# Performance work log

Measured on AMD Instinct MI355X. Metric: run time of the kernel, lower is better.

Reference implementation:

```python
import jax, jax.numpy as jnp
import numpy as np

EPS = 1e-5  # GraphNorm eps


def setup_inputs() -> dict:
    key = jax.random.key(0)
    ks = jax.random.split(key, 8)
    B, N, D, L = 8, 2048, 128, 3
    return {
        "instance": jax.random.uniform(ks[0], (B, N, 2), jnp.float32),
        "Wn": jax.random.normal(ks[1], (D, 2), jnp.float32) * 0.5,
        "bn": jnp.zeros((D,), jnp.float32),
        "Wg": jax.random.normal(ks[2], (L, D, D), jnp.float32) / np.sqrt(D).astype(np.float32),
        "bg": jnp.zeros((L, D), jnp.float32),
        "gn_w": jnp.ones((D,), jnp.float32),
        "gn_b": jnp.zeros((D,), jnp.float32),
        "gn_a": jnp.ones((D,), jnp.float32),
    }


def reference(instance, Wn, bn, Wg, bg, gn_w, gn_b, gn_a):
    # instance: [B, N, 2] city coordinates. Graph is complete, so the PyG
    # edge-list GCN over all (i != j) pairs + self-loops is exactly a dense
    # symmetric-normalized adjacency matmul per graph.
    B, N, _ = instance.shape
    # pairwise Euclidean distances (cdist), safe sqrt to keep diagonal exact 0
    sq = jnp.sum(instance * instance, axis=-1)                      # [B, N]
    d2 = sq[:, :, None] + sq[:, None, :] - 2.0 * jnp.einsum(
        'bnd,bmd->bnm', instance, instance)                          # [B, N, N]
    pos = d2 > 0
    dist = jnp.where(pos, jnp.sqrt(jnp.where(pos, d2, 1.0)), 0.0)    # [B, N, N]
    # GCN edge weights = distances, self-loops added with weight 1.0
    A = dist + jnp.eye(N, dtype=dist.dtype)
    deg = jnp.sum(A, axis=-1)                                        # [B, N]
    dinv = jax.lax.rsqrt(deg)
    An = dinv[:, :, None] * A * dinv[:, None, :]                     # D^-1/2 A D^-1/2

    h = jnp.einsum('bne,de->bnd', instance, Wn) + bn                 # proj_node
    for l in range(Wg.shape[0]):
        # GCNConv: aggregate normalized messages of lin(x), then bias
        hw = jnp.einsum('bnm,bmd->bnd', An, jnp.einsum('bnd,ed->bne', h, Wg[l])) + bg[l]
        h = jnp.tanh(hw) + h                                         # activation + residual
        # GraphNorm (shared params across layers): per-graph, per-feature stats
        mean = jnp.mean(h, axis=1, keepdims=True)                    # [B, 1, D]
        sub = h - gn_a * mean
        var = jnp.mean(sub * sub, axis=1, keepdims=True)
        h = gn_w * sub * jax.lax.rsqrt(var + EPS) + gn_b
    return h  # [B, N, D] (unbatch+stack of equal-size graphs)
```

## Files before the change

kernel.cpp:

```cpp
#include <hip/hip_runtime.h>
#include <hip/hip_bf16.h>
#include <math.h>

#define BB 8
#define NN 2048
#define DD 128
#define LL 3
#define GN_EPS 1e-5f

typedef __attribute__((ext_vector_type(8))) short bf16x8;
typedef __attribute__((ext_vector_type(4))) float f32x4;
typedef __attribute__((ext_vector_type(8))) unsigned short u16x8;

#define FSQRT(x) __builtin_amdgcn_sqrtf(x)

__device__ __forceinline__ unsigned short f2bf(float f) {
    union { float f; unsigned u; } v; v.f = f;
    return (unsigned short)((v.u + 0x8000u) >> 16);
}

__device__ __forceinline__ float fast_tanh(float x) {
    float e = __expf(-2.0f * fabsf(x));
    float t = (1.0f - e) * __builtin_amdgcn_rcpf(1.0f + e);
    return copysignf(t, x);
}

__device__ __forceinline__ void stats_sc(float ps, float pq, float a, float w_,
                                         float b_, float& s, float& c) {
    const float inv_n = 1.0f / (float)NN;
    float mean = ps * inv_n;
    float msq  = pq * inv_n;
    float var  = msq - mean * mean * a * (2.0f - a);
    float rstd = rsqrtf(var + GN_EPS);
    s = w_ * rstd;
    c = b_ - s * (a * mean);
}


__global__ __launch_bounds__(256)
void gen_pack(const float* __restrict__ inst, const float* __restrict__ Wn,
              const float* __restrict__ bn, const float* __restrict__ Wg,
              unsigned short* __restrict__ wgf,
              float* __restrict__ dinv, float* __restrict__ h,
              unsigned short* __restrict__ tp,
              float* __restrict__ psum, float* __restrict__ psq)
{
    __shared__ float cs[NN * 2];
    __shared__ float part[4][16];
    __shared__ float weffL[2 * DD], beffL[DD];
    const int b     = blockIdx.x & 7;
    const int ntile = blockIdx.x >> 3;
    const int n0    = ntile * 16;
    const int tid   = threadIdx.x;
    const int w     = tid >> 6;
    const int lane  = tid & 63;
    const int lq    = lane >> 4;
    const int ll    = lane & 15;

    if (blockIdx.x < 192) {
        const int f = blockIdx.x * 256 + tid;
        const int l  = f >> 14;
        const int r  = f & 16383;
        const int dp = r >> 7;
        const int e  = r & 127;
        const int dpt = dp >> 4, llp = dp & 15;
        const int kc  = e >> 5,  eo = e & 31;
        wgf[((((l * 8 + dpt) * 4 + kc) * 16 + llp) << 5) + eo] = f2bf(Wg[f]);
    }

    const float* instb = inst + b * NN * 2;
    for (int i = tid; i < (NN * 2) / 4; i += 256)
        ((float4*)cs)[i] = ((const float4*)instb)[i];

    if (tid < DD) {
        const int ee = tid;
        float a0 = 0.f, a1 = 0.f, cc = 0.f;
        for (int d = 0; d < 128; ++d) {
            const float wv = Wg[ee * 128 + d];
            a0 = fmaf(wv, Wn[d * 2 + 0], a0);
            a1 = fmaf(wv, Wn[d * 2 + 1], a1);
            cc = fmaf(wv, bn[d], cc);
        }
        weffL[ee * 2 + 0] = a0;
        weffL[ee * 2 + 1] = a1;
        beffL[ee] = cc;
    }
    __syncthreads();

    const int n = n0 + ll;
    const float nx = cs[n * 2 + 0];
    const float ny = cs[n * 2 + 1];

    const int diagkcg = ntile >> 1;
    float rs = 0.f;
    for (int kc = 0; kc < 16; ++kc) {
        const int kcg = w * 16 + kc;
        const int mb  = kcg * 32 + lq * 8;
        const float* cp = &cs[mb * 2];
        float4 c01 = *(const float4*)(cp + 0);
        float4 c23 = *(const float4*)(cp + 4);
        float4 c45 = *(const float4*)(cp + 8);
        float4 c67 = *(const float4*)(cp + 12);
        float mxx[8] = { c01.x, c01.z, c23.x, c23.z, c45.x, c45.z, c67.x, c67.z };
        float myy[8] = { c01.y, c01.w, c23.y, c23.w, c45.y, c45.w, c67.y, c67.w };
        float dist[8];
        #pragma unroll
        for (int j = 0; j < 8; ++j) {
            float dx = nx - mxx[j];
            float dy = ny - myy[j];
            dist[j] = FSQRT(dx * dx + dy * dy);
        }
        if (kcg == diagkcg) {
            #pragma unroll
            for (int j = 0; j < 8; ++j)
                if (mb + j == n) dist[j] = 1.0f;
        }
        #pragma unroll
        for (int j = 0; j < 8; ++j) rs += dist[j];
    }

    rs += __shfl_xor(rs, 16);
    rs += __shfl_xor(rs, 32);
    if (lq == 0) part[w][ll] = rs;
    __syncthreads();
    if (tid < 16)
        dinv[b * NN + n0 + tid] = rsqrtf(part[0][tid] + part[1][tid] +
                                         part[2][tid] + part[3][tid]);

    {
        const int d  = tid & 127;
        const int r0 = tid >> 7;
        const float w0 = Wn[d * 2 + 0];
        const float w1 = Wn[d * 2 + 1];
        const float bv = bn[d];
        const float we0 = weffL[d * 2 + 0];
        const float we1 = weffL[d * 2 + 1];
        const float be  = beffL[d];
        const int kcg   = ntile >> 1;
        const int mbase = (ntile & 1) * 16;
        const int dt    = d >> 4;
        const int lld   = d & 15;
        unsigned short* tpd =
            tp + (((size_t)(b * 64 + kcg) * 8 + dt) * 64 + lld) * 8;
        #pragma unroll
        for (int r = r0; r < 16; r += 2) {
            const float x0 = cs[(n0 + r) * 2 + 0];
            const float x1 = cs[(n0 + r) * 2 + 1];
            h[((size_t)b * NN + n0 + r) * DD + d] = fmaf(x0, w0, fmaf(x1, w1, bv));
            const float dv = rsqrtf(part[0][r] + part[1][r] + part[2][r] + part[3][r]);
            const int mloc = mbase + r;
            const int lqa  = mloc >> 3;
            const int j    = mloc & 7;
            tpd[(size_t)lqa * 128 + j] = f2bf(dv * fmaf(x0, we0, fmaf(x1, we1, be)));
        }
    }
    if (blockIdx.x == 0) {
        for (int i = tid; i < LL * BB * DD; i += 256) { psum[i] = 0.f; psq[i] = 0.f; }
    }
}

template <bool HP>
__global__ __launch_bounds__(256)
void lin_mfma(const float* __restrict__ h, const unsigned short* __restrict__ wgf_l,
              const float* __restrict__ dinv,
              const float* __restrict__ psumP, const float* __restrict__ psqP,
              const float* __restrict__ ga, const float* __restrict__ gw,
              const float* __restrict__ gb, unsigned short* __restrict__ tp)
{
    __shared__ float sL[DD], cL[DD];
    const int tid  = threadIdx.x;
    const int b    = blockIdx.x & 7;
    const int tile = blockIdx.x >> 3;
    const int row0 = b * NN + tile * 32;
    const int w    = tid >> 6;
    const int lane = tid & 63;
    const int lq   = lane >> 4;
    const int ll   = lane & 15;

    if (tid < DD) {
        float s = 1.0f, c = 0.0f;
        if (HP)
            stats_sc(psumP[b * DD + tid], psqP[b * DD + tid],
                     ga[tid], gw[tid], gb[tid], s, c);
        sL[tid] = s; cL[tid] = c;
    }
    __syncthreads();

    bf16x8 aw[2][4];
    #pragma unroll
    for (int mt = 0; mt < 2; ++mt) {
        const int dpt = 2 * w + mt;
        #pragma unroll
        for (int kc = 0; kc < 4; ++kc)
            aw[mt][kc] = *(const bf16x8*)&wgf_l[(((dpt * 4 + kc) * 16 + ll) << 5) + lq * 8];
    }

    bf16x8 bh[2][4];
    #pragma unroll
    for (int nt = 0; nt < 2; ++nt) {
        const float* hrow = h + (size_t)(row0 + nt * 16 + ll) * DD;
        #pragma unroll
        for (int kc = 0; kc < 4; ++kc) {
            float4 h0 = *(const float4*)&hrow[kc * 32 + lq * 8];
            float4 h1 = *(const float4*)&hrow[kc * 32 + lq * 8 + 4];
            const int e0 = kc * 32 + lq * 8;
            bf16x8 p;
            p[0] = (short)f2bf(fmaf(sL[e0 + 0], h0.x, cL[e0 + 0]));
            p[1] = (short)f2bf(fmaf(sL[e0 + 1], h0.y, cL[e0 + 1]));
            p[2] = (short)f2bf(fmaf(sL[e0 + 2], h0.z, cL[e0 + 2]));
            p[3] = (short)f2bf(fmaf(sL[e0 + 3], h0.w, cL[e0 + 3]));
            p[4] = (short)f2bf(fmaf(sL[e0 + 4], h1.x, cL[e0 + 4]));
            p[5] = (short)f2bf(fmaf(sL[e0 + 5], h1.y, cL[e0 + 5]));
            p[6] = (short)f2bf(fmaf(sL[e0 + 6], h1.z, cL[e0 + 6]));
            p[7] = (short)f2bf(fmaf(sL[e0 + 7], h1.w, cL[e0 + 7]));
            bh[nt][kc] = p;
        }
    }

    f32x4 acc[2][2];
    #pragma unroll
    for (int i = 0; i < 2; ++i)
        #pragma unroll
        for (int j = 0; j < 2; ++j) acc[i][j] = (f32x4)0.0f;

    #pragma unroll
    for (int kc = 0; kc < 4; ++kc)
        #pragma unroll
        for (int nt = 0; nt < 2; ++nt)
            #pragma unroll
            for (int mt = 0; mt < 2; ++mt)
                acc[nt][mt] = __builtin_amdgcn_mfma_f32_16x16x32_bf16(
                    bh[nt][kc], aw[mt][kc], acc[nt][mt], 0, 0, 0);

    #pragma unroll
    for (int nt = 0; nt < 2; ++nt) {
        const int mloc0 = nt * 16 + lq * 4;
        const int lq_a  = mloc0 >> 3;
        const int j0    = mloc0 & 7;
        float4 di4 = *(const float4*)&dinv[row0 + mloc0];
        #pragma unroll
        for (int mt = 0; mt < 2; ++mt) {
            const int dt = 2 * w + mt;
            ushort4 pk;
            pk.x = f2bf(acc[nt][mt][0] * di4.x);
            pk.y = f2bf(acc[nt][mt][1] * di4.y);
            pk.z = f2bf(acc[nt][mt][2] * di4.z);
            pk.w = f2bf(acc[nt][mt][3] * di4.w);
            *(ushort4*)&tp[((size_t)((b * 64 + tile) * 8 + dt) * 64 + lq_a * 16 + ll) * 8 + j0] = pk;
        }
    }
}

template <bool HP>
__global__ __launch_bounds__(256, 4)
void agg_mfma(const float* __restrict__ inst, const unsigned short* __restrict__ tp,
              const float* __restrict__ dinv, const float* __restrict__ bg_l,
              const float* __restrict__ psumP, const float* __restrict__ psqP,
              const float* __restrict__ ga, const float* __restrict__ gw,
              const float* __restrict__ gb,
              float* __restrict__ h, float* __restrict__ psum, float* __restrict__ psq)
{
    __shared__ __align__(16) char shm[32768];
    float* cs = (float*)shm;
    const int b     = blockIdx.x & 7;
    const int ntile = blockIdx.x >> 3;
    const int n0    = ntile * 16;
    const int tid   = threadIdx.x;
    const int w     = tid >> 6;
    const int lane  = tid & 63;
    const int lq    = lane >> 4;
    const int ll    = lane & 15;

    const float* instb = inst + b * NN * 2;
    for (int i = tid; i < (NN * 2) / 4; i += 256)
        ((float4*)cs)[i] = ((const float4*)instb)[i];

    const unsigned short* tpb = tp + ((size_t)b * 64 * 8) * 512 + lane * 8;

    f32x4 acc[8];
    #pragma unroll
    for (int dt = 0; dt < 8; ++dt) acc[dt] = (f32x4)0.0f;

    bf16x8 fb[8];

    __syncthreads();

    const int   nr = n0 + ll;
    const float nx = cs[nr * 2 + 0], ny = cs[nr * 2 + 1];
    const int diagk = ntile >> 1;
    const int kcg0  = w * 16;

    #pragma unroll
    for (int kc = 0; kc < 16; ++kc) {
        const int kcg_ = kcg0 + kc;
        #pragma unroll
        for (int dt = 0; dt < 8; ++dt)
            fb[dt] = *(const bf16x8*)(tpb + (size_t)(kcg_ * 8 + dt) * 512);
        const int mb_ = kcg_ * 32 + lq * 8;
        const float* cp_ = &cs[mb_ * 2];
        float4 c01 = *(const float4*)(cp_ + 0);
        float4 c23 = *(const float4*)(cp_ + 4);
        float4 c45 = *(const float4*)(cp_ + 8);
        float4 c67 = *(const float4*)(cp_ + 12);
        float dv[8];
        {
            float mxx[8] = { c01.x, c01.z, c23.x, c23.z, c45.x, c45.z, c67.x, c67.z };
            float myy[8] = { c01.y, c01.w, c23.y, c23.w, c45.y, c45.w, c67.y, c67.w };
            #pragma unroll
            for (int j = 0; j < 8; ++j) {
                float dx = nx - mxx[j], dy = ny - myy[j];
                dv[j] = FSQRT(dx * dx + dy * dy);
            }
        }
        if (kcg_ == diagk) {
            #pragma unroll
            for (int j = 0; j < 8; ++j)
                if (mb_ + j == nr) dv[j] = 1.0f;
        }
        bf16x8 af;
        #pragma unroll
        for (int j = 0; j < 8; ++j) af[j] = (short)f2bf(dv[j]);
        #pragma unroll
        for (int dt = 0; dt < 8; ++dt)
            acc[dt] = __builtin_amdgcn_mfma_f32_16x16x32_bf16(fb[dt], af, acc[dt], 0, 0, 0);
    }

    __syncthreads();
    #pragma unroll
    for (int dt = 0; dt < 8; ++dt)
        *(f32x4*)(shm + ((dt * 4 + w) * 1024) + lane * 16) = acc[dt];
    __syncthreads();

    f32x4 accs[2];
    #pragma unroll
    for (int dtl = 0; dtl < 2; ++dtl) {
        const int dt = 2 * w + dtl;
        f32x4 r0 = *(const f32x4*)(shm + ((dt * 4 + 0) * 1024) + lane * 16);
        f32x4 r1 = *(const f32x4*)(shm + ((dt * 4 + 1) * 1024) + lane * 16);
        f32x4 r2 = *(const f32x4*)(shm + ((dt * 4 + 2) * 1024) + lane * 16);
        f32x4 r3 = *(const f32x4*)(shm + ((dt * 4 + 3) * 1024) + lane * 16);
        accs[dtl] = ((r0 + r1) + r2) + r3;
    }

    const float di = dinv[b * NN + nr];
    #pragma unroll
    for (int dtl = 0; dtl < 2; ++dtl) {
        const int d0 = (2 * w + dtl) * 16 + lq * 4;
        float4 bg4 = *(const float4*)&bg_l[d0];
        float sres[4] = {1.f, 1.f, 1.f, 1.f}, cres[4] = {0.f, 0.f, 0.f, 0.f};
        if (HP) {
            float4 ps4 = *(const float4*)&psumP[b * DD + d0];
            float4 pq4 = *(const float4*)&psqP[b * DD + d0];
            float4 ga4 = *(const float4*)&ga[d0];
            float4 gw4 = *(const float4*)&gw[d0];
            float4 gb4 = *(const float4*)&gb[d0];
            stats_sc(ps4.x, pq4.x, ga4.x, gw4.x, gb4.x, sres[0], cres[0]);
            stats_sc(ps4.y, pq4.y, ga4.y, gw4.y, gb4.y, sres[1], cres[1]);
            stats_sc(ps4.z, pq4.z, ga4.z, gw4.z, gb4.z, sres[2], cres[2]);
            stats_sc(ps4.w, pq4.w, ga4.w, gw4.w, gb4.w, sres[3], cres[3]);
        }
        size_t idx = ((size_t)b * NN + nr) * DD + d0;
        float4 hv = *(const float4*)&h[idx];
        float outv[4];
        float hs[4], hq[4];
        #pragma unroll
        for (int r = 0; r < 4; ++r) {
            float pre = di * accs[dtl][r] + (&bg4.x)[r];
            outv[r] = fast_tanh(pre) + fmaf(sres[r], (&hv.x)[r], cres[r]);
            hs[r] = outv[r];
            hq[r] = outv[r] * outv[r];
        }
        float4 ov = { outv[0], outv[1], outv[2], outv[3] };
        *(float4*)&h[idx] = ov;

        #pragma unroll
        for (int off = 1; off < 16; off <<= 1) {
            #pragma unroll
            for (int r = 0; r < 4; ++r) {
                hs[r] += __shfl_xor(hs[r], off);
                hq[r] += __shfl_xor(hq[r], off);
            }
        }
        if (ll == 0) {
            #pragma unroll
            for (int r = 0; r < 4; ++r) {
                atomicAdd(&psum[b * DD + d0 + r], hs[r]);
                atomicAdd(&psq[b * DD + d0 + r], hq[r]);
            }
        }
    }
}

__global__ __launch_bounds__(256)
void apply_kernel(const float* __restrict__ h,
                  const float* __restrict__ psum2, const float* __restrict__ psq2,
                  const float* __restrict__ ga, const float* __restrict__ gw,
                  const float* __restrict__ gb, float* __restrict__ dst)
{
    const int i4 = blockIdx.x * 256 + threadIdx.x;
    const int dg = (i4 & 31) * 4;
    const int b  = i4 >> 16;
    float4 hv = ((const float4*)h)[i4];
    float o[4];
    #pragma unroll
    for (int j = 0; j < 4; ++j) {
        const int d = dg + j;
        float s, c;
        stats_sc(psum2[b * DD + d], psq2[b * DD + d], ga[d], gw[d], gb[d], s, c);
        o[j] = fmaf(s, (&hv.x)[j], c);
    }
    float4 ov = { o[0], o[1], o[2], o[3] };
    ((float4*)dst)[i4] = ov;
}

extern "C" void kernel_launch(void* const* d_in, const int* in_sizes, int n_in,
                              void* d_out, int out_size, void* d_ws, size_t ws_size,
                              hipStream_t stream)
{
    const float* inst = (const float*)d_in[0];
    const float* Wn   = (const float*)d_in[1];
    const float* bn   = (const float*)d_in[2];
    const float* Wg   = (const float*)d_in[3];
    const float* bg   = (const float*)d_in[4];
    const float* gw   = (const float*)d_in[5];
    const float* gb   = (const float*)d_in[6];
    const float* ga   = (const float*)d_in[7];
    float* out = (float*)d_out;

    float* ws   = (float*)d_ws;
    float* dinv = ws;
    float* h    = dinv + BB * NN;
    float* psum = h + (size_t)BB * NN * DD;
    float* psq  = psum + LL * BB * DD;
    unsigned short* wgf = (unsigned short*)(psq + LL * BB * DD);
    unsigned short* tp  = wgf + LL * DD * DD;

    gen_pack<<<1024, 256, 0, stream>>>(inst, Wn, bn, Wg, wgf, dinv, h, tp, psum, psq);

    agg_mfma<false><<<1024, 256, 0, stream>>>(
        inst, tp, dinv, bg + 0 * DD, nullptr, nullptr, ga, gw, gb, h, psum, psq);

    for (int l = 1; l < LL; ++l) {
        const unsigned short* wgl = wgf + (size_t)l * DD * DD;
        const float* psP = psum + (size_t)(l - 1) * BB * DD;
        const float* pqP = psq  + (size_t)(l - 1) * BB * DD;
        float* psL = psum + (size_t)l * BB * DD;
        float* pqL = psq  + (size_t)l * BB * DD;
        lin_mfma<true><<<(BB * NN) / 32, 256, 0, stream>>>(
            h, wgl, dinv, psP, pqP, ga, gw, gb, tp);
        agg_mfma<true><<<1024, 256, 0, stream>>>(
            inst, tp, dinv, bg + l * DD, psP, pqP, ga, gw, gb, h, psL, pqL);
    }
    apply_kernel<<<(BB * NN * DD / 4) / 256, 256, 0, stream>>>(
        h, psum + 2 * BB * DD, psq + 2 * BB * DD, ga, gw, gb, out);
}
```

Baseline: 196.8 us.

## Process two 16-row tiles per block in aggregation to reuse packed B fragments

```diff
diff --git a/kernel.cpp b/kernel.cpp
--- a/kernel.cpp
+++ b/kernel.cpp
@@ -252,7 +252,7 @@
 }
 
 template <bool HP>
-__global__ __launch_bounds__(256, 4)
+__global__ __launch_bounds__(512, 4)
 void agg_mfma(const float* __restrict__ inst, const unsigned short* __restrict__ tp,
               const float* __restrict__ dinv, const float* __restrict__ bg_l,
               const float* __restrict__ psumP, const float* __restrict__ psqP,
@@ -260,133 +260,164 @@
               const float* __restrict__ gb,
               float* __restrict__ h, float* __restrict__ psum, float* __restrict__ psq)
 {
-    __shared__ __align__(16) char shm[32768];
-    float* cs = (float*)shm;
-    const int b     = blockIdx.x & 7;
-    const int ntile = blockIdx.x >> 3;
-    const int n0    = ntile * 16;
-    const int tid   = threadIdx.x;
-    const int w     = tid >> 6;
-    const int lane  = tid & 63;
-    const int lq    = lane >> 4;
-    const int ll    = lane & 15;
+    __shared__ float cs[NN * 2];
+    __shared__ __align__(16) char red[32768];
+    const int b    = blockIdx.x & 7;
+    const int t2   = blockIdx.x >> 3;
+    const int n0   = t2 * 32;
+    const int tid  = threadIdx.x;
+    const int w    = tid >> 6;
+    const int lane = tid & 63;
+    const int lq   = lane >> 4;
+    const int ll   = lane & 15;
 
     const float* instb = inst + b * NN * 2;
-    for (int i = tid; i < (NN * 2) / 4; i += 256)
+    for (int i = tid; i < (NN * 2) / 4; i += 512)
         ((float4*)cs)[i] = ((const float4*)instb)[i];
 
     const unsigned short* tpb = tp + ((size_t)b * 64 * 8) * 512 + lane * 8;
 
-    f32x4 acc[8];
-    #pragma unroll
-    for (int dt = 0; dt < 8; ++dt) acc[dt] = (f32x4)0.0f;
-
-    bf16x8 fb[8];
+    f32x4 acc[2][8];
+    #pragma unroll
+    for (int nt = 0; nt < 2; ++nt)
+        #pragma unroll
+        for (int dt = 0; dt < 8; ++dt) acc[nt][dt] = (f32x4)0.0f;
+
+    bf16x8 fb[4];
 
     __syncthreads();
 
-    const int   nr = n0 + ll;
-    const float nx = cs[nr * 2 + 0], ny = cs[nr * 2 + 1];
-    const int diagk = ntile >> 1;
-    const int kcg0  = w * 16;
-
-    #pragma unroll
-    for (int kc = 0; kc < 16; ++kc) {
+    const int   nr0 = n0 + ll;
+    const int   nr1 = n0 + 16 + ll;
+    const float nx0 = cs[nr0 * 2 + 0], ny0 = cs[nr0 * 2 + 1];
+    const float nx1 = cs[nr1 * 2 + 0], ny1 = cs[nr1 * 2 + 1];
+
+    const int kcg0 = w * 8;
+
+    #pragma unroll
+    for (int kc = 0; kc < 8; ++kc) {
         const int kcg_ = kcg0 + kc;
         #pragma unroll
-        for (int dt = 0; dt < 8; ++dt)
-            fb[dt] = *(const bf16x8*)(tpb + (size_t)(kcg_ * 8 + dt) * 512);
+        for (int i = 0; i < 4; ++i)
+            fb[i] = *(const bf16x8*)(tpb + (size_t)(kcg_ * 8 + i) * 512);
+
         const int mb_ = kcg_ * 32 + lq * 8;
         const float* cp_ = &cs[mb_ * 2];
         float4 c01 = *(const float4*)(cp_ + 0);
         float4 c23 = *(const float4*)(cp_ + 4);
         float4 c45 = *(const float4*)(cp_ + 8);
         float4 c67 = *(const float4*)(cp_ + 12);
-        float dv[8];
+        float dv0[8], dv1[8];
         {
             float mxx[8] = { c01.x, c01.z, c23.x, c23.z, c45.x, c45.z, c67.x, c67.z };
             float myy[8] = { c01.y, c01.w, c23.y, c23.w, c45.y, c45.w, c67.y, c67.w };
             #pragma unroll
             for (int j = 0; j < 8; ++j) {
-                float dx = nx - mxx[j], dy = ny - myy[j];
-                dv[j] = FSQRT(dx * dx + dy * dy);
+                float dx0 = nx0 - mxx[j], dy0 = ny0 - myy[j];
+                dv0[j] = FSQRT(dx0 * dx0 + dy0 * dy0);
+                float dx1 = nx1 - mxx[j], dy1 = ny1 - myy[j];
+                dv1[j] = FSQRT(dx1 * dx1 + dy1 * dy1);
             }
         }
-        if (kcg_ == diagk) {
+        if (kcg_ == t2) {
             #pragma unroll
-            for (int j = 0; j < 8; ++j)
-                if (mb_ + j == nr) dv[j] = 1.0f;
-        }
-        bf16x8 af;
-        #pragma unroll
-        for (int j = 0; j < 8; ++j) af[j] = (short)f2bf(dv[j]);
-        #pragma unroll
-        for (int dt = 0; dt < 8; ++dt)
-            acc[dt] = __builtin_amdgcn_mfma_f32_16x16x32_bf16(fb[dt], af, acc[dt], 0, 0, 0);
-    }
-
+            for (int j = 0; j < 8; ++j) {
+                if (mb_ + j == nr0) dv0[j] = 1.0f;
+                if (mb_ + j == nr1) dv1[j] = 1.0f;
+            }
+        }
+        bf16x8 af0, af1;
+        #pragma unroll
+        for (int j = 0; j < 8; ++j) {
+            af0[j] = (short)f2bf(dv0[j]);
+            af1[j] = (short)f2bf(dv1[j]);
+        }
+
+        #pragma unroll
+        for (int i = 0; i < 4; ++i) {
+            acc[0][i] = __builtin_amdgcn_mfma_f32_16x16x32_bf16(fb[i], af0, acc[0][i], 0, 0, 0);
+            acc[1][i] = __builtin_amdgcn_mfma_f32_16x16x32_bf16(fb[i], af1, acc[1][i], 0, 0, 0);
+        }
+        #pragma unroll
+        for (int i = 0; i < 4; ++i)
+            fb[i] = *(const bf16x8*)(tpb + (size_t)(kcg_ * 8 + 4 + i) * 512);
+        #pragma unroll
+        for (int i = 0; i < 4; ++i) {
+            acc[0][4 + i] = __builtin_amdgcn_mfma_f32_16x16x32_bf16(fb[i], af0, acc[0][4 + i], 0, 0, 0);
+            acc[1][4 + i] = __builtin_amdgcn_mfma_f32_16x16x32_bf16(fb[i], af1, acc[1][4 + i], 0, 0, 0);
+        }
+    }
+
+    f32x4 accs[2];
+    #pragma unroll
+    for (int nt = 0; nt < 2; ++nt) {
+        #pragma unroll
+        for (int dh = 0; dh < 2; ++dh) {
+            __syncthreads();
+            #pragma unroll
+            for (int dtl = 0; dtl < 4; ++dtl)
+                *(f32x4*)(red + ((dtl * 8 + w) * 1024) + lane * 16) = acc[nt][dh * 4 + dtl];
+            __syncthreads();
+            if ((w >> 2) == dh) {
+                const int dtl = w & 3;
+                f32x4 s = *(const f32x4*)(red + ((dtl * 8 + 0) * 1024) + lane * 16);
+                #pragma unroll
+                for (int ww = 1; ww < 8; ++ww)
+                    s = s + *(const f32x4*)(red + ((dtl * 8 + ww) * 1024) + lane * 16);
+                accs[nt] = s;
+            }
+        }
+    }
     __syncthreads();
-    #pragma unroll
-    for (int dt = 0; dt < 8; ++dt)
-        *(f32x4*)(shm + ((dt * 4 + w) * 1024) + lane * 16) = acc[dt];
-    __syncthreads();
-
-    f32x4 accs[2];
-    #pragma unroll
-    for (int dtl = 0; dtl < 2; ++dtl) {
-        const int dt = 2 * w + dtl;
-        f32x4 r0 = *(const f32x4*)(shm + ((dt * 4 + 0) * 1024) + lane * 16);
-        f32x4 r1 = *(const f32x4*)(shm + ((dt * 4 + 1) * 1024) + lane * 16);
-        f32x4 r2 = *(const f32x4*)(shm + ((dt * 4 + 2) * 1024) + lane * 16);
-        f32x4 r3 = *(const f32x4*)(shm + ((dt * 4 + 3) * 1024) + lane * 16);
-        accs[dtl] = ((r0 + r1) + r2) + r3;
-    }
-
-    const float di = dinv[b * NN + nr];
-    #pragma unroll
-    for (int dtl = 0; dtl < 2; ++dtl) {
-        const int d0 = (2 * w + dtl) * 16 + lq * 4;
-        float4 bg4 = *(const float4*)&bg_l[d0];
-        float sres[4] = {1.f, 1.f, 1.f, 1.f}, cres[4] = {0.f, 0.f, 0.f, 0.f};
-        if (HP) {
-            float4 ps4 = *(const float4*)&psumP[b * DD + d0];
-            float4 pq4 = *(const float4*)&psqP[b * DD + d0];
-            float4 ga4 = *(const float4*)&ga[d0];
-            float4 gw4 = *(const float4*)&gw[d0];
-            float4 gb4 = *(const float4*)&gb[d0];
-            stats_sc(ps4.x, pq4.x, ga4.x, gw4.x, gb4.x, sres[0], cres[0]);
-            stats_sc(ps4.y, pq4.y, ga4.y, gw4.y, gb4.y, sres[1], cres[1]);
-            stats_sc(ps4.z, pq4.z, ga4.z, gw4.z, gb4.z, sres[2], cres[2]);
-            stats_sc(ps4.w, pq4.w, ga4.w, gw4.w, gb4.w, sres[3], cres[3]);
-        }
-        size_t idx = ((size_t)b * NN + nr) * DD + d0;
+
+    const int d0 = w * 16 + lq * 4;
+    const float di0 = dinv[b * NN + nr0];
+    const float di1 = dinv[b * NN + nr1];
+    float4 bg4 = *(const float4*)&bg_l[d0];
+    float sres[4] = {1.f, 1.f, 1.f, 1.f}, cres[4] = {0.f, 0.f, 0.f, 0.f};
+    if (HP) {
+        float4 ps4 = *(const float4*)&psumP[b * DD + d0];
+        float4 pq4 = *(const float4*)&psqP[b * DD + d0];
+        float4 ga4 = *(const float4*)&ga[d0];
+        float4 gw4 = *(const float4*)&gw[d0];
+        float4 gb4 = *(const float4*)&gb[d0];
+        stats_sc(ps4.x, pq4.x, ga4.x, gw4.x, gb4.x, sres[0], cres[0]);
+        stats_sc(ps4.y, pq4.y, ga4.y, gw4.y, gb4.y, sres[1], cres[1]);
+        stats_sc(ps4.z, pq4.z, ga4.z, gw4.z, gb4.z, sres[2], cres[2]);
+        stats_sc(ps4.w, pq4.w, ga4.w, gw4.w, gb4.w, sres[3], cres[3]);
+    }
+    float hs[4] = {0.f, 0.f, 0.f, 0.f}, hq[4] = {0.f, 0.f, 0.f, 0.f};
+    #pragma unroll
+    for (int nt = 0; nt < 2; ++nt) {
+        const int n = nt ? nr1 : nr0;
+        const float di = nt ? di1 : di0;
+        size_t idx = ((size_t)b * NN + n) * DD + d0;
         float4 hv = *(const float4*)&h[idx];
         float outv[4];
-        float hs[4], hq[4];
         #pragma unroll
         for (int r = 0; r < 4; ++r) {
-            float pre = di * accs[dtl][r] + (&bg4.x)[r];
+            float pre = di * accs[nt][r] + (&bg4.x)[r];
             outv[r] = fast_tanh(pre) + fmaf(sres[r], (&hv.x)[r], cres[r]);
-            hs[r] = outv[r];
-            hq[r] = outv[r] * outv[r];
+            hs[r] += outv[r];
+            hq[r] += outv[r] * outv[r];
         }
         float4 ov = { outv[0], outv[1], outv[2], outv[3] };
         *(float4*)&h[idx] = ov;
-
-        #pragma unroll
-        for (int off = 1; off < 16; off <<= 1) {
-            #pragma unroll
-            for (int r = 0; r < 4; ++r) {
-                hs[r] += __shfl_xor(hs[r], off);
-                hq[r] += __shfl_xor(hq[r], off);
-            }
-        }
-        if (ll == 0) {
-            #pragma unroll
-            for (int r = 0; r < 4; ++r) {
-                atomicAdd(&psum[b * DD + d0 + r], hs[r]);
-                atomicAdd(&psq[b * DD + d0 + r], hq[r]);
-            }
+    }
+
+    #pragma unroll
+    for (int off = 1; off < 16; off <<= 1) {
+        #pragma unroll
+        for (int r = 0; r < 4; ++r) {
+            hs[r] += __shfl_xor(hs[r], off);
+            hq[r] += __shfl_xor(hq[r], off);
+        }
+    }
+    if (ll == 0) {
+        #pragma unroll
+        for (int r = 0; r < 4; ++r) {
+            atomicAdd(&psum[b * DD + d0 + r], hs[r]);
+            atomicAdd(&psq[b * DD + d0 + r], hq[r]);
         }
     }
 }
@@ -437,7 +468,7 @@
 
     gen_pack<<<1024, 256, 0, stream>>>(inst, Wn, bn, Wg, wgf, dinv, h, tp, psum, psq);
 
-    agg_mfma<false><<<1024, 256, 0, stream>>>(
+    agg_mfma<false><<<512, 512, 0, stream>>>(
         inst, tp, dinv, bg + 0 * DD, nullptr, nullptr, ga, gw, gb, h, psum, psq);
 
     for (int l = 1; l < LL; ++l) {
@@ -448,7 +479,7 @@
         float* pqL = psq  + (size_t)l * BB * DD;
         lin_mfma<true><<<(BB * NN) / 32, 256, 0, stream>>>(
             h, wgl, dinv, psP, pqP, ga, gw, gb, tp);
-        agg_mfma<true><<<1024, 256, 0, stream>>>(
+        agg_mfma<true><<<512, 512, 0, stream>>>(
             inst, tp, dinv, bg + l * DD, psP, pqP, ga, gw, gb, h, psL, pqL);
     }
     apply_kernel<<<(BB * NN * DD / 4) / 256, 256, 0, stream>>>(
```

Measured after the change: 187.8 us. 4.5% less time.
